# Performance work log

Hardware: AMD Instinct MI355X
Metric: run time of the kernel (lower is better)

## Reference

```python
import jax, jax.numpy as jnp
import numpy as np

K_NEIGHBORS = 32
BN_EPS = 1e-5


def setup_inputs() -> dict:
    key = jax.random.key(0)
    ks = jax.random.split(key, 5)
    B, N, C, OUT = 16, 2048, 3, 32
    x = jax.random.normal(ks[0], (B, N, C), dtype=jnp.float32)
    W1 = jax.random.normal(ks[1], (2 * C, 2 * C), dtype=jnp.float32) * 0.3
    b1 = jax.random.normal(ks[2], (2 * C,), dtype=jnp.float32) * 0.05
    W2 = jax.random.normal(ks[3], (2 * C, OUT), dtype=jnp.float32) * 0.3
    b2 = jax.random.normal(ks[4], (OUT,), dtype=jnp.float32) * 0.05
    return {
        "x": x,
        "W1": W1, "b1": b1,
        "gamma1": jnp.ones((2 * C,), jnp.float32), "beta1": jnp.zeros((2 * C,), jnp.float32),
        "W2": W2, "b2": b2,
        "gamma2": jnp.ones((OUT,), jnp.float32), "beta2": jnp.zeros((OUT,), jnp.float32),
    }


def _batchnorm_train(h, gamma, beta):
    # normalize over all axes except the last (channel) axis, biased variance
    axes = tuple(range(h.ndim - 1))
    mean = jnp.mean(h, axis=axes)
    var = jnp.var(h, axis=axes)
    return gamma * (h - mean) * jax.lax.rsqrt(var + BN_EPS) + beta


def reference(x, W1, b1, gamma1, beta1, W2, b2, gamma2, beta2):
    B, N, C = x.shape
    K = min(K_NEIGHBORS, N)
    # brute-force KNN: squared euclidean distances [B,N,N]
    sq = jnp.sum(x * x, axis=-1)
    d = sq[:, :, None] + sq[:, None, :] - 2.0 * jnp.einsum('bnc,bmc->bnm', x, x)
    _, idx = jax.lax.top_k(-d, K)  # [B,N,K] nearest (self first)
    # gather neighbor points: [B,N,K,C]
    knn = jax.vmap(lambda pts, i: pts[i])(x, idx)
    diffs = x[:, :, None, :] - knn
    h = jnp.concatenate([jnp.broadcast_to(x[:, :, None, :], (B, N, K, C)), diffs], axis=-1)  # [B,N,K,2C]
    h = jax.nn.elu(_batchnorm_train(h @ W1 + b1, gamma1, beta1))
    h = jnp.max(h, axis=2)  # max-pool over K neighbors -> [B,N,2C]
    y = jax.nn.elu(_batchnorm_train(h @ W2 + b2, gamma2, beta2))
    return y
```

## Files before the change

kernel.cpp:

```cpp
#include <hip/hip_runtime.h>
#include <math.h>

namespace {
constexpr int NB = 16, NP = 2048, KNN = 32, CH1 = 6, CH2 = 32;
constexpr int QPB = 8;
constexpr int NBLK = NB * NP / QPB;
constexpr float BN_EPS = 1e-5f;

constexpr size_t OFF_S1REP   = 0;
constexpr size_t OFF_STATS2L = 768;
constexpr size_t OFF_SC1     = 1664;
constexpr size_t OFF_P       = 2048;
constexpr size_t OFF_MINQ    = OFF_P + sizeof(float)*NB*NP*CH1;
}

typedef __attribute__((ext_vector_type(2))) float f32x2;

__device__ __forceinline__ f32x2 pk_mul(f32x2 a, f32x2 b) {
  f32x2 d; asm("v_pk_mul_f32 %0, %1, %2" : "=v"(d) : "v"(a), "v"(b)); return d;
}
__device__ __forceinline__ f32x2 pk_add(f32x2 a, f32x2 b) {
  f32x2 d; asm("v_pk_add_f32 %0, %1, %2" : "=v"(d) : "v"(a), "v"(b)); return d;
}

template <int C> __device__ __forceinline__ int dpp0i(int x) {
  return __builtin_amdgcn_update_dpp(0, x, C, 0xf, 0xf, true);
}
template <int C, int RM> __device__ __forceinline__ int dpp0i_rm(int x) {
  return __builtin_amdgcn_update_dpp(0, x, C, RM, 0xf, true);
}
template <int C> __device__ __forceinline__ float dpp0f(float x) {
  return __uint_as_float((unsigned)__builtin_amdgcn_update_dpp(
      0, (int)__float_as_uint(x), C, 0xf, 0xf, true));
}
template <int C> __device__ __forceinline__ float dppInff(float x) {
  return __uint_as_float((unsigned)__builtin_amdgcn_update_dpp(
      0x7F800000, (int)__float_as_uint(x), C, 0xf, 0xf, false));
}
__device__ __forceinline__ int wave_isum_bcast(int x) {
  x += dpp0i<0x111>(x); x += dpp0i<0x112>(x); x += dpp0i<0x114>(x);
  x += dpp0i<0x118>(x); x += dpp0i<0x142>(x); x += dpp0i<0x143>(x);
  return __builtin_amdgcn_readlane(x, 63);
}
__device__ __forceinline__ int wave_iscan_incl(int x) {
  x += dpp0i<0x111>(x); x += dpp0i<0x112>(x); x += dpp0i<0x114>(x);
  x += dpp0i<0x118>(x);
  x += dpp0i_rm<0x142, 0xa>(x);
  x += dpp0i_rm<0x143, 0xc>(x);
  return x;
}
__device__ __forceinline__ float wave_fsum63(float x) {
  x += dpp0f<0x111>(x); x += dpp0f<0x112>(x); x += dpp0f<0x114>(x);
  x += dpp0f<0x118>(x); x += dpp0f<0x142>(x); x += dpp0f<0x143>(x);
  return x;
}
__device__ __forceinline__ float wave_fmin63(float x) {
  x = fminf(x, dppInff<0x111>(x)); x = fminf(x, dppInff<0x112>(x));
  x = fminf(x, dppInff<0x114>(x)); x = fminf(x, dppInff<0x118>(x));
  x = fminf(x, dppInff<0x142>(x)); x = fminf(x, dppInff<0x143>(x));
  return x;
}

#define BSEL(m, x, y) ((((x)) & (m)) | (((y)) & ~(m)))

__global__ __launch_bounds__(512, 4) void knn_kernel(const float* __restrict__ x,
                                                     const float* __restrict__ W1,
                                                     const float* __restrict__ b1,
                                                     float* __restrict__ pout,
                                                     float* __restrict__ minq,
                                                     double* __restrict__ s1rep) {
  __shared__ float4 XC[512], YC[512], ZC[512], WC[512];
  __shared__ float XP[2048], YP[2048], ZP[2048];
  __shared__ float red[12][QPB];
  const int lane = threadIdx.x & 63;
  const int w    = threadIdx.x >> 6;
  const int qi   = blockIdx.x * QPB + w;
  const int b    = qi >> 11;
  const int n    = qi & (NP - 1);

  const float* xb = x + (size_t)b * NP * 3;
  {
    const int t = threadIdx.x;
    const float4* g4 = (const float4*)xb;
    float4 f0 = g4[t*3], f1 = g4[t*3+1], f2 = g4[t*3+2];
    float4 X = {f0.x, f0.w, f1.z, f2.y};
    float4 Y = {f0.y, f1.x, f1.w, f2.z};
    float4 Z = {f0.z, f1.y, f2.x, f2.w};
    float4 Wv;
    Wv.x = __fadd_rn(__fadd_rn(__fmul_rn(X.x,X.x), __fmul_rn(Y.x,Y.x)), __fmul_rn(Z.x,Z.x));
    Wv.y = __fadd_rn(__fadd_rn(__fmul_rn(X.y,X.y), __fmul_rn(Y.y,Y.y)), __fmul_rn(Z.y,Z.y));
    Wv.z = __fadd_rn(__fadd_rn(__fmul_rn(X.z,X.z), __fmul_rn(Y.z,Y.z)), __fmul_rn(Z.z,Z.z));
    Wv.w = __fadd_rn(__fadd_rn(__fmul_rn(X.w,X.w), __fmul_rn(Y.w,Y.w)), __fmul_rn(Z.w,Z.w));
    const int cs = (t & 7) * 64 + (t >> 3);
    XC[cs] = X; YC[cs] = Y; ZC[cs] = Z; WC[cs] = Wv;
    const int l0 = t >> 3, vb = (t & 7) * 4;
    XP[(vb+0)*64+l0] = X.x; XP[(vb+1)*64+l0] = X.y; XP[(vb+2)*64+l0] = X.z; XP[(vb+3)*64+l0] = X.w;
    YP[(vb+0)*64+l0] = Y.x; YP[(vb+1)*64+l0] = Y.y; YP[(vb+2)*64+l0] = Y.z; YP[(vb+3)*64+l0] = Y.w;
    ZP[(vb+0)*64+l0] = Z.x; ZP[(vb+1)*64+l0] = Z.y; ZP[(vb+2)*64+l0] = Z.z; ZP[(vb+3)*64+l0] = Z.w;
  }
  __syncthreads();

  const int ln = n >> 5, vn = n & 31;
  const float qx = XP[vn*64 + ln], qy = YP[vn*64 + ln], qz = ZP[vn*64 + ln];
  const float qw = ((const float*)WC)[((vn >> 2)*64 + ln)*4 + (vn & 3)];
  const f32x2 qx2 = {qx,qx}, qy2 = {qy,qy}, qz2 = {qz,qz}, qw2 = {qw,qw};

  unsigned dd[32];
#pragma unroll
  for (int g = 0; g < 8; ++g) {
    const int cs = g*64 + lane;
    float4 X = XC[cs], Y = YC[cs], Z = ZC[cs], Wv = WC[cs];
    f32x2 x01 = {X.x,X.y}, y01 = {Y.x,Y.y}, z01 = {Z.x,Z.y}, w01 = {Wv.x,Wv.y};
    f32x2 x23 = {X.z,X.w}, y23 = {Y.z,Y.w}, z23 = {Z.z,Z.w}, w23 = {Wv.z,Wv.w};
    f32x2 dotA = pk_add(pk_add(pk_mul(qx2,x01), pk_mul(qy2,y01)), pk_mul(qz2,z01));
    f32x2 dotB = pk_add(pk_add(pk_mul(qx2,x23), pk_mul(qy2,y23)), pk_mul(qz2,z23));
    f32x2 ssA = pk_add(qw2, w01), ssB = pk_add(qw2, w23);
    f32x2 dA = pk_add(dotA, dotA), dB = pk_add(dotB, dotB);
    dd[31-(4*g+0)] = __float_as_uint(__fsub_rn(ssA.x, dA.x));
    dd[31-(4*g+1)] = __float_as_uint(__fsub_rn(ssA.y, dA.y));
    dd[31-(4*g+2)] = __float_as_uint(__fsub_rn(ssB.x, dB.x));
    dd[31-(4*g+3)] = __float_as_uint(__fsub_rn(ssB.y, dB.y));
  }

  unsigned h[16], l[16];
#pragma unroll
  for (int g = 0; g < 16; ++g) {
    h[g] = __builtin_amdgcn_perm(dd[g], dd[g+16], 0x07060302u);
    l[g] = __builtin_amdgcn_perm(dd[g], dd[g+16], 0x05040100u);
  }
#pragma unroll
  for (int g = 0; g < 8; ++g) {
    unsigned hi = h[g], lo = h[g+8];
    h[g]   = __builtin_amdgcn_perm(hi, lo, 0x07030501u);
    h[g+8] = __builtin_amdgcn_perm(hi, lo, 0x06020400u);
  }
#pragma unroll
  for (int g = 0; g < 8; ++g) {
    int k = (g >> 2)*8 + (g & 3);
    unsigned A = h[k], B = h[k+4];
    h[k]   = BSEL(0x0F0F0F0Fu, B >> 4, A);
    h[k+4] = BSEL(0xF0F0F0F0u, A << 4, B);
  }
#pragma unroll
  for (int g = 0; g < 8; ++g) {
    int k = (g >> 1)*4 + (g & 1);
    unsigned A = h[k], B = h[k+2];
    h[k]   = BSEL(0x33333333u, B >> 2, A);
    h[k+2] = BSEL(0xCCCCCCCCu, A << 2, B);
  }
#pragma unroll
  for (int g = 0; g < 8; ++g) {
    int k = g*2;
    unsigned A = h[k], B = h[k+1];
    h[k]   = BSEL(0x55555555u, B >> 1, A);
    h[k+1] = BSEL(0xAAAAAAAAu, A << 1, B);
  }

  unsigned alive = 0xFFFFFFFFu, below = 0u;
  int rem = KNN, ca = 2048;
#pragma unroll
  for (int i = 1; i <= 6; ++i) {
    unsigned zeros = BSEL(h[i], 0u, alive);
    int c0 = wave_isum_bcast(__popc(zeros));
    if (c0 >= rem) { alive = zeros; ca = c0; }
    else { rem -= c0; below |= zeros; alive &= h[i]; ca -= c0; }
  }
#pragma unroll
  for (int i = 7; i <= 15; ++i) {
    if (ca != rem) {
      unsigned zeros = BSEL(h[i], 0u, alive);
      int c0 = wave_isum_bcast(__popc(zeros));
      if (c0 >= rem) { alive = zeros; ca = c0; }
      else { rem -= c0; below |= zeros; alive &= h[i]; ca -= c0; }
    }
  }
  unsigned sel;
  if (__builtin_expect(ca == rem, 1)) {
    sel = below | alive;
  } else {
#pragma unroll
    for (int g = 0; g < 8; ++g) {
      unsigned hi = l[g], lo = l[g+8];
      l[g]   = __builtin_amdgcn_perm(hi, lo, 0x07030501u);
      l[g+8] = __builtin_amdgcn_perm(hi, lo, 0x06020400u);
    }
#pragma unroll
    for (int g = 0; g < 8; ++g) {
      int k = (g >> 2)*8 + (g & 3);
      unsigned A = l[k], B = l[k+4];
      l[k]   = BSEL(0x0F0F0F0Fu, B >> 4, A);
      l[k+4] = BSEL(0xF0F0F0F0u, A << 4, B);
    }
#pragma unroll
    for (int g = 0; g < 8; ++g) {
      int k = (g >> 1)*4 + (g & 1);
      unsigned A = l[k], B = l[k+2];
      l[k]   = BSEL(0x33333333u, B >> 2, A);
      l[k+2] = BSEL(0xCCCCCCCCu, A << 2, B);
    }
#pragma unroll
    for (int g = 0; g < 8; ++g) {
      int k = g*2;
      unsigned A = l[k], B = l[k+1];
      l[k]   = BSEL(0x55555555u, B >> 1, A);
      l[k+1] = BSEL(0xAAAAAAAAu, A << 1, B);
    }
#pragma unroll
    for (int i = 0; i < 16; ++i) {
      if (ca != rem) {
        unsigned zeros = BSEL(l[i], 0u, alive);
        int c0 = wave_isum_bcast(__popc(zeros));
        if (c0 >= rem) { alive = zeros; ca = c0; }
        else { rem -= c0; below |= zeros; alive &= l[i]; ca -= c0; }
      }
    }
    sel = below;
    if (ca == rem) {
      sel |= alive;
    } else {
      int cnt  = __popc(alive);
      int excl = wave_iscan_incl(cnt) - cnt;
      int k = rem - excl;
      k = k < 0 ? 0 : (k > cnt ? cnt : k);
      while (k > 0) {
        unsigned bb = alive & (unsigned)(-(int)alive);
        sel |= bb; alive ^= bb; --k;
      }
    }
  }

  float w3[CH1], w4[CH1], w5[CH1];
#pragma unroll
  for (int c = 0; c < CH1; ++c) { w3[c]=W1[3*CH1+c]; w4[c]=W1[4*CH1+c]; w5[c]=W1[5*CH1+c]; }
  float sq_[CH1], sqq[CH1], mn[CH1];
#pragma unroll
  for (int c = 0; c < CH1; ++c) { sq_[c] = 0.f; sqq[c] = 0.f; mn[c] = INFINITY; }
  unsigned m = sel;
  while (m) {
    int v = __builtin_ctz(m); m &= m - 1;
    int s = (v << 6) | lane;
    float px_ = XP[s], py_ = YP[s], pz_ = ZP[s];
#pragma unroll
    for (int c = 0; c < CH1; ++c) {
      float qv = px_*w3[c] + py_*w4[c] + pz_*w5[c];
      sq_[c] += qv; sqq[c] += qv*qv; mn[c] = fminf(mn[c], qv);
    }
  }

  float pv[CH1];
#pragma unroll
  for (int c = 0; c < CH1; ++c) {
    float qv = qx*w3[c] + qy*w4[c] + qz*w5[c];
    pv[c] = b1[c] + qx*W1[c] + qy*W1[CH1+c] + qz*W1[2*CH1+c] + qv;
  }

#pragma unroll
  for (int c = 0; c < CH1; ++c) {
    float s  = wave_fsum63(sq_[c]);
    float s2 = wave_fsum63(sqq[c]);
    float mm = wave_fmin63(mn[c]);
    if (lane == 63) {
      minq[qi*CH1 + c] = mm;
      red[c][w]       = fmaf(32.f, pv[c], -s);
      red[CH1 + c][w] = fmaf(32.f, pv[c]*pv[c], fmaf(-2.f*pv[c], s, s2));
    }
  }
  if (lane == 0) {
#pragma unroll
    for (int c = 0; c < CH1; ++c) pout[qi*CH1 + c] = pv[c];
  }
  __syncthreads();
  if (threadIdx.x < 12) {
    float s = 0.f;
#pragma unroll
    for (int ww = 0; ww < QPB; ++ww) s += red[threadIdx.x][ww];
    atomicAdd(s1rep + (blockIdx.x & 7) * 12 + threadIdx.x, (double)s);
  }
}

__global__ __launch_bounds__(256) void stage2_kernel(const float* __restrict__ p,
                                                     const float* __restrict__ minq,
                                                     const double* __restrict__ s1rep,
                                                     const float* __restrict__ gamma1,
                                                     const float* __restrict__ beta1,
                                                     float* __restrict__ sc1g,
                                                     double* __restrict__ stats2L) {
  __shared__ double tot1[12];
  __shared__ float sc1s[12];
  __shared__ float acc[4][27];
  const int t = threadIdx.x;
  if (t < 12) {
    double s = 0.0;
#pragma unroll
    for (int r = 0; r < 8; ++r) s += s1rep[r*12 + t];
    tot1[t] = s;
  }
  __syncthreads();
  if (t < CH1) {
    double cnt  = (double)NB * NP * KNN;
    double mean = tot1[t] / cnt;
    double var  = tot1[CH1 + t] / cnt - mean * mean;
    float scale = gamma1[t] / sqrtf((float)var + BN_EPS);
    sc1s[t] = scale; sc1s[CH1 + t] = beta1[t] - (float)mean * scale;
  }
  __syncthreads();
  if (blockIdx.x == 0 && t < 12) sc1g[t] = sc1s[t];

  const int qi = blockIdx.x * 256 + t;
  const int w = t >> 6, lane = t & 63;
  float me[CH1];
#pragma unroll
  for (int c = 0; c < CH1; ++c) {
    float v = fmaf(sc1s[c], p[qi*CH1 + c] - minq[qi*CH1 + c], sc1s[CH1 + c]);
    me[c] = v > 0.f ? v : expm1f(v);
  }
  float vals[27];
#pragma unroll
  for (int c = 0; c < CH1; ++c) vals[c] = me[c];
  {
    int id = 6;
#pragma unroll
    for (int c = 0; c < CH1; ++c)
#pragma unroll
      for (int d = c; d < CH1; ++d) { vals[id] = me[c]*me[d]; ++id; }
  }
#pragma unroll
  for (int k = 0; k < 27; ++k) {
    float s = wave_fsum63(vals[k]);
    if (lane == 63) acc[w][k] = s;
  }
  __syncthreads();
  if (t < 27)
    atomicAdd(stats2L + (blockIdx.x & 3) * 27 + t,
              (double)((acc[0][t] + acc[1][t]) + (acc[2][t] + acc[3][t])));
}

__global__ __launch_bounds__(256) void out_kernel(const float* __restrict__ p,
                                                  const float* __restrict__ minq,
                                                  const float* __restrict__ sc1,
                                                  const float* __restrict__ W2,
                                                  const float* __restrict__ b2,
                                                  const double* __restrict__ stats2L,
                                                  const float* __restrict__ gamma2,
                                                  const float* __restrict__ beta2,
                                                  float* __restrict__ out) {
  __shared__ float m2[27];
  __shared__ float me_lds[8][CH1];
  __shared__ float s2s[CH2], s2h[CH2];
  const int t = threadIdx.x;
  if (t < 27)
    m2[t] = (float)(((stats2L[t] + stats2L[27+t]) + (stats2L[54+t] + stats2L[81+t])));
  const int qbase = blockIdx.x * 8;
  if (t >= 64 && t < 112) {
    int qs = (t - 64) / 6, c = (t - 64) % 6;
    int qi = qbase + qs;
    float v = fmaf(sc1[c], p[qi*CH1 + c] - minq[qi*CH1 + c], sc1[CH1 + c]);
    me_lds[qs][c] = v > 0.f ? v : expm1f(v);
  }
  __syncthreads();
  if (t < CH2) {
    float wv[CH1];
#pragma unroll
    for (int c = 0; c < CH1; ++c) wv[c] = W2[c*CH2 + t];
    float sy = 0.f;
#pragma unroll
    for (int c = 0; c < CH1; ++c) sy = fmaf(wv[c], m2[c], sy);
    float sy2 = 0.f;
    {
      int id = 6;
#pragma unroll
      for (int c = 0; c < CH1; ++c)
#pragma unroll
        for (int d = c; d < CH1; ++d) {
          float coef = (c == d) ? wv[c]*wv[c] : 2.f*wv[c]*wv[d];
          sy2 = fmaf(coef, m2[id], sy2); ++id;
        }
    }
    const double N = (double)NB * NP;
    double bo   = (double)b2[t];
    double mean = ((double)sy + N*bo) / N;
    double Ey2  = ((double)sy2 + 2.0*bo*(double)sy + N*bo*bo) / N;
    double var  = Ey2 - mean*mean;
    float scale = gamma2[t] / sqrtf((float)var + BN_EPS);
    s2s[t] = scale; s2h[t] = beta2[t] - (float)mean * scale;
  }
  __syncthreads();
  const int qs = t >> 5, o = t & 31;
  const int qi = qbase + qs;
  float y = b2[o];
#pragma unroll
  for (int c = 0; c < CH1; ++c) y = fmaf(me_lds[qs][c], W2[c*CH2 + o], y);
  float r = fmaf(s2s[o], y, s2h[o]);
  out[(size_t)qi*CH2 + o] = r > 0.f ? r : expm1f(r);
}

extern "C" void kernel_launch(void* const* d_in, const int* in_sizes, int n_in,
                              void* d_out, int out_size, void* d_ws, size_t ws_size,
                              hipStream_t stream) {
  const float* x      = (const float*)d_in[0];
  const float* W1     = (const float*)d_in[1];
  const float* b1     = (const float*)d_in[2];
  const float* gamma1 = (const float*)d_in[3];
  const float* beta1  = (const float*)d_in[4];
  const float* W2     = (const float*)d_in[5];
  const float* b2     = (const float*)d_in[6];
  const float* gamma2 = (const float*)d_in[7];
  const float* beta2  = (const float*)d_in[8];
  float* out = (float*)d_out;
  char* ws = (char*)d_ws;

  double* s1rep   = (double*)(ws + OFF_S1REP);
  double* stats2L = (double*)(ws + OFF_STATS2L);
  float* sc1  = (float*)(ws + OFF_SC1);
  float* p    = (float*)(ws + OFF_P);
  float* minq = (float*)(ws + OFF_MINQ);

  hipMemsetAsync(ws, 0, 1664, stream);

  knn_kernel   <<<dim3(NBLK),       dim3(512), 0, stream>>>(x, W1, b1, p, minq, s1rep);
  stage2_kernel<<<dim3(NB*NP/256),  dim3(256), 0, stream>>>(p, minq, s1rep, gamma1, beta1,
                                                            sc1, stats2L);
  out_kernel   <<<dim3(NB*NP/8),    dim3(256), 0, stream>>>(p, minq, sc1, W2, b2,
                                                            stats2L, gamma2, beta2, out);
}
```

Baseline: 85.04 us.

## Drop duplicate planar LDS copy, remap point layout, raise occupancy hint

Removes the separate XP/YP/ZP shared arrays and stores points only in the float4 XC/YC/ZC/WC arrays, with a new index mapping used for the query, the distance loop and the neighbor gather. This cuts shared memory per block (about 24KB less), and the launch bound rises from 4 to 6 blocks per CU to use that headroom. The tie-break selection switches from a DPP prefix scan plus a per-lane loop to a ballot-per-bit loop. Global loads become strided scalar loads instead of float4 loads, and the tighter register limit may cause spills.

```diff
diff --git a/kernel.cpp b/kernel.cpp
--- a/kernel.cpp
+++ b/kernel.cpp
@@ -26,9 +26,6 @@
 template <int C> __device__ __forceinline__ int dpp0i(int x) {
   return __builtin_amdgcn_update_dpp(0, x, C, 0xf, 0xf, true);
 }
-template <int C, int RM> __device__ __forceinline__ int dpp0i_rm(int x) {
-  return __builtin_amdgcn_update_dpp(0, x, C, RM, 0xf, true);
-}
 template <int C> __device__ __forceinline__ float dpp0f(float x) {
   return __uint_as_float((unsigned)__builtin_amdgcn_update_dpp(
       0, (int)__float_as_uint(x), C, 0xf, 0xf, true));
@@ -41,13 +38,6 @@
   x += dpp0i<0x111>(x); x += dpp0i<0x112>(x); x += dpp0i<0x114>(x);
   x += dpp0i<0x118>(x); x += dpp0i<0x142>(x); x += dpp0i<0x143>(x);
   return __builtin_amdgcn_readlane(x, 63);
-}
-__device__ __forceinline__ int wave_iscan_incl(int x) {
-  x += dpp0i<0x111>(x); x += dpp0i<0x112>(x); x += dpp0i<0x114>(x);
-  x += dpp0i<0x118>(x);
-  x += dpp0i_rm<0x142, 0xa>(x);
-  x += dpp0i_rm<0x143, 0xc>(x);
-  return x;
 }
 __device__ __forceinline__ float wave_fsum63(float x) {
   x += dpp0f<0x111>(x); x += dpp0f<0x112>(x); x += dpp0f<0x114>(x);
@@ -63,14 +53,13 @@
 
 #define BSEL(m, x, y) ((((x)) & (m)) | (((y)) & ~(m)))
 
-__global__ __launch_bounds__(512, 4) void knn_kernel(const float* __restrict__ x,
+__global__ __launch_bounds__(512, 6) void knn_kernel(const float* __restrict__ x,
                                                      const float* __restrict__ W1,
                                                      const float* __restrict__ b1,
                                                      float* __restrict__ pout,
                                                      float* __restrict__ minq,
                                                      double* __restrict__ s1rep) {
   __shared__ float4 XC[512], YC[512], ZC[512], WC[512];
-  __shared__ float XP[2048], YP[2048], ZP[2048];
   __shared__ float red[12][QPB];
   const int lane = threadIdx.x & 63;
   const int w    = threadIdx.x >> 6;
@@ -81,28 +70,30 @@
   const float* xb = x + (size_t)b * NP * 3;
   {
     const int t = threadIdx.x;
-    const float4* g4 = (const float4*)xb;
-    float4 f0 = g4[t*3], f1 = g4[t*3+1], f2 = g4[t*3+2];
-    float4 X = {f0.x, f0.w, f1.z, f2.y};
-    float4 Y = {f0.y, f1.x, f1.w, f2.z};
-    float4 Z = {f0.z, f1.y, f2.x, f2.w};
-    float4 Wv;
-    Wv.x = __fadd_rn(__fadd_rn(__fmul_rn(X.x,X.x), __fmul_rn(Y.x,Y.x)), __fmul_rn(Z.x,Z.x));
-    Wv.y = __fadd_rn(__fadd_rn(__fmul_rn(X.y,X.y), __fmul_rn(Y.y,Y.y)), __fmul_rn(Z.y,Z.y));
-    Wv.z = __fadd_rn(__fadd_rn(__fmul_rn(X.z,X.z), __fmul_rn(Y.z,Y.z)), __fmul_rn(Z.z,Z.z));
-    Wv.w = __fadd_rn(__fadd_rn(__fmul_rn(X.w,X.w), __fmul_rn(Y.w,Y.w)), __fmul_rn(Z.w,Z.w));
-    const int cs = (t & 7) * 64 + (t >> 3);
-    XC[cs] = X; YC[cs] = Y; ZC[cs] = Z; WC[cs] = Wv;
-    const int l0 = t >> 3, vb = (t & 7) * 4;
-    XP[(vb+0)*64+l0] = X.x; XP[(vb+1)*64+l0] = X.y; XP[(vb+2)*64+l0] = X.z; XP[(vb+3)*64+l0] = X.w;
-    YP[(vb+0)*64+l0] = Y.x; YP[(vb+1)*64+l0] = Y.y; YP[(vb+2)*64+l0] = Y.z; YP[(vb+3)*64+l0] = Y.w;
-    ZP[(vb+0)*64+l0] = Z.x; ZP[(vb+1)*64+l0] = Z.y; ZP[(vb+2)*64+l0] = Z.z; ZP[(vb+3)*64+l0] = Z.w;
-  }
-  __syncthreads();
-
-  const int ln = n >> 5, vn = n & 31;
-  const float qx = XP[vn*64 + ln], qy = YP[vn*64 + ln], qz = ZP[vn*64 + ln];
-  const float qw = ((const float*)WC)[((vn >> 2)*64 + ln)*4 + (vn & 3)];
+    const int g0 = t >> 6, ls = t & 63;
+    float xx[4], yy[4], zz[4], ww[4];
+#pragma unroll
+    for (int k = 0; k < 4; ++k) {
+      const float* pp = xb + (g0*256 + k*64 + ls) * 3;
+      float a0 = pp[0], a1 = pp[1], a2 = pp[2];
+      xx[k] = a0; yy[k] = a1; zz[k] = a2;
+      ww[k] = __fadd_rn(__fadd_rn(__fmul_rn(a0,a0), __fmul_rn(a1,a1)), __fmul_rn(a2,a2));
+    }
+    XC[t] = (float4){xx[0], xx[1], xx[2], xx[3]};
+    YC[t] = (float4){yy[0], yy[1], yy[2], yy[3]};
+    ZC[t] = (float4){zz[0], zz[1], zz[2], zz[3]};
+    WC[t] = (float4){ww[0], ww[1], ww[2], ww[3]};
+  }
+  __syncthreads();
+
+  const float* Xs = (const float*)XC;
+  const float* Ys = (const float*)YC;
+  const float* Zs = (const float*)ZC;
+  const float* Ws = (const float*)WC;
+
+  const int vq = n >> 6, lq = n & 63;
+  const int qidx = (((vq >> 2) << 6) | lq) * 4 + (vq & 3);
+  const float qx = Xs[qidx], qy = Ys[qidx], qz = Zs[qidx], qw = Ws[qidx];
   const f32x2 qx2 = {qx,qx}, qy2 = {qy,qy}, qz2 = {qz,qz}, qw2 = {qw,qw};
 
   unsigned dd[32];
@@ -218,13 +209,16 @@
     if (ca == rem) {
       sel |= alive;
     } else {
-      int cnt  = __popc(alive);
-      int excl = wave_iscan_incl(cnt) - cnt;
-      int k = rem - excl;
-      k = k < 0 ? 0 : (k > cnt ? cnt : k);
-      while (k > 0) {
-        unsigned bb = alive & (unsigned)(-(int)alive);
-        sel |= bb; alive ^= bb; --k;
+      for (int v = 0; v < 32; ++v) {
+        if (rem <= 0) break;
+        bool mine = (alive >> v) & 1;
+        unsigned long long mb = __ballot(mine);
+        int c = __popcll(mb);
+        if (c <= rem) { if (mine) sel |= 1u << v; rem -= c; }
+        else {
+          if (mine && (int)__popcll(mb & ((1ull << lane) - 1)) < rem) sel |= 1u << v;
+          rem = 0;
+        }
       }
     }
   }
@@ -238,8 +232,8 @@
   unsigned m = sel;
   while (m) {
     int v = __builtin_ctz(m); m &= m - 1;
-    int s = (v << 6) | lane;
-    float px_ = XP[s], py_ = YP[s], pz_ = ZP[s];
+    int idx = (((v >> 2) << 6) | lane) * 4 + (v & 3);
+    float px_ = Xs[idx], py_ = Ys[idx], pz_ = Zs[idx];
 #pragma unroll
     for (int c = 0; c < CH1; ++c) {
       float qv = px_*w3[c] + py_*w4[c] + pz_*w5[c];
@@ -273,7 +267,7 @@
   if (threadIdx.x < 12) {
     float s = 0.f;
 #pragma unroll
-    for (int ww = 0; ww < QPB; ++ww) s += red[threadIdx.x][ww];
+    for (int ww2 = 0; ww2 < QPB; ++ww2) s += red[threadIdx.x][ww2];
     atomicAdd(s1rep + (blockIdx.x & 7) * 12 + threadIdx.x, (double)s);
   }
 }
```

Measured after the change: 72.04 us, median of 2. 15.3% less time.
